# Performance work log

Hardware: AMD Instinct MI355X
Metric: run time of the kernel (lower is better)

Reference implementation:

```python
import jax, jax.numpy as jnp
import numpy as np

D = 256      # input_size == output_size
H = 8        # head_count
DH = D // H  # dim per head


def setup_inputs() -> dict:
    key = jax.random.key(0)
    ks = jax.random.split(key, 11)
    s = 1.0 / np.sqrt(D)
    inp = {
        "x": jax.random.normal(ks[0], (4, 2048, D), dtype=jnp.float32),
        "Wq": jax.random.normal(ks[1], (D, D), dtype=jnp.float32) * s,
        "bq": jnp.zeros((D,), jnp.float32),
        "Wk": jax.random.normal(ks[2], (D, D), dtype=jnp.float32) * s,
        "bk": jnp.zeros((D,), jnp.float32),
        "Wv": jax.random.normal(ks[3], (D, D), dtype=jnp.float32) * s,
        "bv": jnp.zeros((D,), jnp.float32),
        "Wo": jax.random.normal(ks[4], (D, D), dtype=jnp.float32) * s,
        "bo": jnp.zeros((D,), jnp.float32),
        "Wc": jax.random.normal(ks[5], (D, D), dtype=jnp.float32) * s,
        "bc": jnp.zeros((D,), jnp.float32),
    }
    return inp


def _split_heads(t):
    b, n, _ = t.shape
    return t.reshape(b, n, H, DH).transpose(0, 2, 1, 3)  # b h n dh


def reference(x, Wq, bq, Wk, bk, Wv, bv, Wo, bo, Wc, bc):
    # Multi-head self-attention over all nodes (complete graph)
    q = _split_heads(x @ Wq + bq)
    k = _split_heads(x @ Wk + bk)
    v = _split_heads(x @ Wv + bv)
    scale = 1.0 / jnp.sqrt(jnp.asarray(DH, x.dtype))
    scores = jnp.einsum("bhqd,bhkd->bhqk", q * scale, k)
    attn = jax.nn.softmax(scores, axis=-1)  # attn dropout = identity (eval)
    ctx = jnp.einsum("bhqk,bhkd->bhqd", attn, v)
    b, _, n, _ = ctx.shape
    ctx = ctx.transpose(0, 2, 1, 3).reshape(b, n, D)
    ctx = ctx @ Wo + bo  # MHA output projection
    # linear_context + dropout (identity in eval) + residual
    out = x + (ctx @ Wc + bc)
    return out
```

## Files before the change

### kernel.cpp

```cpp
#include <hip/hip_runtime.h>

#define DMODEL 256
#define HEADS 8
#define DHEAD 32
#define NSEQ 2048
#define BATCH 4
#define MTOT (BATCH*NSEQ)

typedef __bf16 bf16x8 __attribute__((ext_vector_type(8)));
typedef float f32x4 __attribute__((ext_vector_type(4)));

#define CS 0.25507282111989365f

__device__ __forceinline__ unsigned short f2bf(float f) {
    union { float f; unsigned int u; } v; v.f = f;
    unsigned int u = v.u;
    unsigned int r = u + 0x7FFFu + ((u >> 16) & 1u);
    return (unsigned short)(r >> 16);
}

__device__ __forceinline__ unsigned pkbf(float a, float b) {
    union { __bf16 h[2]; unsigned u; } t;
    t.h[0] = (__bf16)a; t.h[1] = (__bf16)b;
    return t.u;
}

__device__ __forceinline__ f32x4 mfma16(bf16x8 a, bf16x8 b, f32x4 c) {
    return __builtin_amdgcn_mfma_f32_16x16x32_bf16(a, b, c, 0, 0, 0);
}

#define GLD16(g, l) __builtin_amdgcn_global_load_lds( \
    (const __attribute__((address_space(1))) unsigned int*)(g), \
    (__attribute__((address_space(3))) unsigned int*)(l), 16, 0, 0)

__global__ __launch_bounds__(256) void prep_kernel(
    const float* __restrict__ x,
    const float* __restrict__ Wq, const float* __restrict__ Wk,
    const float* __restrict__ Wv, const float* __restrict__ Wo,
    const float* __restrict__ Wc,
    const float* __restrict__ bq, const float* __restrict__ bk,
    const float* __restrict__ bv, const float* __restrict__ bo,
    const float* __restrict__ bc,
    unsigned short* __restrict__ xbf,
    unsigned short* __restrict__ Wt,
    float* __restrict__ bcat,
    unsigned short* __restrict__ Woct,
    float* __restrict__ bocf)
{
    const int tid = threadIdx.x;
    if (blockIdx.x < 257) {
        int k = blockIdx.x;
        int n = tid;
        const float* arow = (k < 256) ? (Wo + k * 256) : bo;
        float a0 = 0.f, a1 = 0.f, a2 = 0.f, a3 = 0.f;
#pragma unroll 4
        for (int j = 0; j < 256; j += 4) {
            a0 = fmaf(arow[j],     Wc[j * 256 + n],       a0);
            a1 = fmaf(arow[j + 1], Wc[(j + 1) * 256 + n], a1);
            a2 = fmaf(arow[j + 2], Wc[(j + 2) * 256 + n], a2);
            a3 = fmaf(arow[j + 3], Wc[(j + 3) * 256 + n], a3);
        }
        float acc = (a0 + a1) + (a2 + a3);
        if (k < 256) Woct[n * 256 + k] = f2bf(acc);
        else         bocf[n] = acc + bc[n];
        return;
    }
    if (blockIdx.x < 2305) {
        int idx = (blockIdx.x - 257) * 256 + tid;
        float4 v = reinterpret_cast<const float4*>(x)[idx];
        ushort4 o;
        o.x = f2bf(v.x); o.y = f2bf(v.y); o.z = f2bf(v.z); o.w = f2bf(v.w);
        reinterpret_cast<ushort4*>(xbf)[idx] = o;
        return;
    }
    if (blockIdx.x < 2385) {
        __shared__ unsigned short Lt[64 * 72];
        const int bb = blockIdx.x - 2305;
        const int wid = tid >> 6, lane = tid & 63;
        const int n0 = (bb >> 2) * 64, k0 = (bb & 3) * 64;
        const float* Wsrc; int col0;
        if (n0 < 256)       { Wsrc = Wq; col0 = n0; }
        else if (n0 < 512)  { Wsrc = Wk; col0 = n0 - 256; }
        else if (n0 < 768)  { Wsrc = Wv; col0 = n0 - 512; }
        else if (n0 < 1024) { Wsrc = Wo; col0 = n0 - 768; }
        else                { Wsrc = Wc; col0 = n0 - 1024; }
#pragma unroll
        for (int r = 0; r < 16; ++r) {
            int k = k0 + wid * 16 + r;
            Lt[lane * 72 + wid * 16 + r] = f2bf(Wsrc[k * 256 + col0 + lane]);
        }
        __syncthreads();
#pragma unroll
        for (int c = tid; c < 512; c += 256) {
            int row = c >> 3, seg = c & 7;
            *reinterpret_cast<bf16x8*>(Wt + (n0 + row) * 256 + k0 + seg * 8) =
                *reinterpret_cast<const bf16x8*>(Lt + row * 72 + seg * 8);
        }
        return;
    }
    int t = (blockIdx.x - 2385) * 256 + tid;
    if (t < 1280) {
        float v;
        if (t < 256)       v = bq[t];
        else if (t < 512)  v = bk[t - 256];
        else if (t < 768)  v = bv[t - 512];
        else if (t < 1024) v = bo[t - 768];
        else               v = bc[t - 1024];
        bcat[t] = v;
    }
}

__global__ __launch_bounds__(256) void gemm_qkv(
    const unsigned short* __restrict__ A,
    const unsigned short* __restrict__ Wt,
    const float* __restrict__ bias,
    unsigned short* __restrict__ outQ,
    unsigned short* __restrict__ outK,
    unsigned short* __restrict__ outVt)
{
    __shared__ __align__(16) unsigned short Bl[64 * 256];
    const int tid = threadIdx.x;
    const int wid = tid >> 6;
    const int lane = tid & 63;
    const int lo = lane & 15, hi = lane >> 4;
    const int m0 = blockIdx.x * 128 + wid * 32;
    const int n0 = blockIdx.y * 64;

#pragma unroll
    for (int j = 0; j < 8; ++j) {
        int chunkbase = (j * 4 + wid) * 64;
        int chunk = chunkbase + lane;
        int row = chunk >> 5, Jp = chunk & 31;
        int J = (Jp & 24) | ((Jp ^ row) & 7);
        GLD16(Wt + (n0 + row) * 256 + J * 8, Bl + chunkbase * 8);
    }
    asm volatile("s_waitcnt vmcnt(0)" ::: "memory");
    __syncthreads();

    const unsigned short* arow0 = A + (m0 + lo) * 256 + hi * 8;
    f32x4 acc[2][4] = {};
#pragma unroll
    for (int s = 0; s < 8; ++s) {
        bf16x8 a0 = *reinterpret_cast<const bf16x8*>(arow0 + s * 32);
        bf16x8 a1 = *reinterpret_cast<const bf16x8*>(arow0 + 16 * 256 + s * 32);
        int Jp = ((s >> 1) << 3) | ((((s & 1) << 2) + hi) ^ (lo & 7));
#pragma unroll
        for (int n = 0; n < 4; ++n) {
            bf16x8 b = *reinterpret_cast<const bf16x8*>(
                Bl + (n * 16 + lo) * 256 + Jp * 8);
            acc[0][n] = mfma16(a0, b, acc[0][n]);
            acc[1][n] = mfma16(a1, b, acc[1][n]);
        }
    }

    const int type = blockIdx.y >> 2;
    const int m0b = blockIdx.x * 128;
    unsigned short* Lb = Bl;
    __syncthreads();
    if (type < 2) {
#pragma unroll
        for (int mf = 0; mf < 2; ++mf)
#pragma unroll
        for (int n = 0; n < 4; ++n) {
            float bs = bias[n0 + n * 16 + lo];
#pragma unroll
            for (int i = 0; i < 4; ++i) {
                float val = acc[mf][n][i] + bs;
                if (type == 0) val *= CS;
                Lb[(wid * 32 + mf * 16 + hi * 4 + i) * 72 + n * 16 + lo] = f2bf(val);
            }
        }
    } else {
#pragma unroll
        for (int mf = 0; mf < 2; ++mf)
#pragma unroll
        for (int n = 0; n < 4; ++n) {
            float bs = bias[n0 + n * 16 + lo];
            uint2 pk;
            pk.x = pkbf(acc[mf][n][0] + bs, acc[mf][n][1] + bs);
            pk.y = pkbf(acc[mf][n][2] + bs, acc[mf][n][3] + bs);
            *reinterpret_cast<uint2*>(
                Lb + (n * 16 + lo) * 136 + wid * 32 + mf * 16 + hi * 4) = pk;
        }
    }
    __syncthreads();
    if (type < 2) {
        unsigned short* outP = (type == 0) ? outQ : outK;
#pragma unroll
        for (int r = 0; r < 4; ++r) {
            int cid = r * 256 + tid;
            int m_l = cid >> 3, seg = cid & 7;
            bf16x8 chunk = *reinterpret_cast<const bf16x8*>(Lb + m_l * 72 + seg * 8);
            int m = m0b + m_l, gc = n0 + seg * 8;
            int b = m >> 11, nn = m & 2047, hh = (gc >> 5) & 7, dh = gc & 31;
            *reinterpret_cast<bf16x8*>(
                outP + (((b * 8) + hh) * 2048 + nn) * 32 + dh) = chunk;
        }
    } else {
#pragma unroll
        for (int r = 0; r < 4; ++r) {
            int cid = r * 256 + tid;
            int gcl = cid >> 4, seg = cid & 15;
            const unsigned short* src = Lb + gcl * 136 + seg * 8;
            uint2 lo4 = *reinterpret_cast<const uint2*>(src);
            uint2 hi4 = *reinterpret_cast<const uint2*>(src + 4);
            int gc = n0 + gcl, m = m0b + seg * 8;
            int b = m >> 11, nn = m & 2047, hh = (gc >> 5) & 7, dh = gc & 31;
            int pos0 = (nn & ~63) | (nn & 32) | ((nn & 8) << 1) | ((nn & 16) >> 2);
            unsigned short* dst = outVt + (((b * 8) + hh) * 32 + dh) * 2048;
            *reinterpret_cast<uint2*>(dst + pos0)     = lo4;
            *reinterpret_cast<uint2*>(dst + pos0 + 8) = hi4;
        }
    }
}

__global__ __launch_bounds__(256, 4) void attn_kernel(
    const unsigned short* __restrict__ Q,
    const unsigned short* __restrict__ K,
    const unsigned short* __restrict__ Vt,
    unsigned short* __restrict__ ctx)
{
    __shared__ __align__(16) char smem[32768];

    const int tid = threadIdx.x;
    const int wid = tid >> 6;
    const int lane = tid & 63;
    const int lo = lane & 15, hi = lane >> 4;

    const int bid = blockIdx.x;
    const int bh = ((bid >> 7) << 3) | (bid & 7);
    const int qt = (bid >> 3) & 15;
    const int q0 = qt * 128 + wid * 32;

    const unsigned short* Qb = Q + bh * (NSEQ * 32);
    const unsigned short* Kb = K + bh * (NSEQ * 32);
    const unsigned short* Vb = Vt + bh * (32 * NSEQ);

    bf16x8 qfA = *reinterpret_cast<const bf16x8*>(Qb + (q0 + lo) * 32 + hi * 8);
    bf16x8 qfB = *reinterpret_cast<const bf16x8*>(Qb + (q0 + 16 + lo) * 32 + hi * 8);

    const int lt = tid;
    const unsigned short* ksrc0 = Kb + (2 * (lt >> 3) + ((lt >> 2) & 1)) * 32
                                     + ((lt & 3) ^ ((lt >> 3) & 3)) * 8;
    const unsigned short* ksrc1 = ksrc0 + 64 * 32;
    const unsigned short* vsrc0 = Vb + (lt >> 3) * NSEQ
                                     + ((lt & 7) ^ ((lt >> 3) & 7)) * 8;
    const unsigned short* vsrc1 = vsrc0 + 64;
    char* kdst = smem + lt * 16;
    char* vdst = smem + 16384 + lt * 16;

    f32x4 o0A = {}, o1A = {}, odA = {};
    f32x4 o0B = {}, o1B = {}, odB = {};
    const f32x4 z = {};
    const int prs = lo & 7;
    const int kxor = (hi ^ ((lo >> 1) & 3)) * 8;

    union { unsigned u[4]; bf16x8 v; } ones;
    ones.u[0] = 0x3F803F80u; ones.u[1] = 0x3F803F80u;
    ones.u[2] = 0x3F803F80u; ones.u[3] = 0x3F803F80u;

#define STAGE_T(tt, buf) do { \
    GLD16(ksrc0 + (tt) * 4096, kdst + (buf) * 8192); \
    GLD16(ksrc1 + (tt) * 4096, kdst + (buf) * 8192 + 4096); \
    GLD16(vsrc0 + (tt) * 128,  vdst + (buf) * 8192); \
    GLD16(vsrc1 + (tt) * 128,  vdst + (buf) * 8192 + 4096); \
} while (0)

#define PVKK(S0, S1, T0, T1, A0, A1) do { \
    union { unsigned u[4]; bf16x8 v; } pbA; \
    pbA.u[0] = pkbf(__builtin_amdgcn_exp2f(S0[0]), __builtin_amdgcn_exp2f(S0[1])); \
    pbA.u[1] = pkbf(__builtin_amdgcn_exp2f(S0[2]), __builtin_amdgcn_exp2f(S0[3])); \
    pbA.u[2] = pkbf(__builtin_amdgcn_exp2f(S1[0]), __builtin_amdgcn_exp2f(S1[1])); \
    pbA.u[3] = pkbf(__builtin_amdgcn_exp2f(S1[2]), __builtin_amdgcn_exp2f(S1[3])); \
    union { unsigned u[4]; bf16x8 v; } pbB; \
    pbB.u[0] = pkbf(__builtin_amdgcn_exp2f(T0[0]), __builtin_amdgcn_exp2f(T0[1])); \
    pbB.u[1] = pkbf(__builtin_amdgcn_exp2f(T0[2]), __builtin_amdgcn_exp2f(T0[3])); \
    pbB.u[2] = pkbf(__builtin_amdgcn_exp2f(T1[0]), __builtin_amdgcn_exp2f(T1[1])); \
    pbB.u[3] = pkbf(__builtin_amdgcn_exp2f(T1[2]), __builtin_amdgcn_exp2f(T1[3])); \
    o0A = mfma16(A0, pbA.v, o0A); \
    o1A = mfma16(A1, pbA.v, o1A); \
    odA = mfma16(ones.v, pbA.v, odA); \
    o0B = mfma16(A0, pbB.v, o0B); \
    o1B = mfma16(A1, pbB.v, o1B); \
    odB = mfma16(ones.v, pbB.v, odB); \
} while (0)

    STAGE_T(0, 0);
    asm volatile("s_waitcnt vmcnt(0)" ::: "memory");
    __builtin_amdgcn_s_barrier();
    __builtin_amdgcn_sched_barrier(0);

    int cur = 0;
    for (int t = 0; t < 16; ++t) {
        if (t < 15) STAGE_T(t + 1, cur ^ 1);
        const unsigned short* Kc = (const unsigned short*)(smem + cur * 8192);
        const unsigned short* Vc = (const unsigned short*)(smem + 16384 + cur * 8192);

        __builtin_amdgcn_s_setprio(1);
#pragma unroll
        for (int h2 = 0; h2 < 2; ++h2) {
            const unsigned short* Kh = Kc + h2 * 2048;
            const unsigned short* Vh = Vc + h2 * 2048;
            f32x4 sA[4], sB[4];
#pragma unroll
            for (int c = 0; c < 4; ++c) {
                bf16x8 kf = *reinterpret_cast<const bf16x8*>(
                    Kh + (c * 16 + lo) * 32 + kxor);
                sA[c] = mfma16(kf, qfA, z);
                sB[c] = mfma16(kf, qfB, z);
            }
#pragma unroll
            for (int kk = 0; kk < 2; ++kk) {
                int sw = ((4 * kk + hi) ^ prs) * 8;
                bf16x8 a0 = *reinterpret_cast<const bf16x8*>(Vh + lo * 64 + sw);
                bf16x8 a1 = *reinterpret_cast<const bf16x8*>(Vh + (16 + lo) * 64 + sw);
                PVKK(sA[2 * kk], sA[2 * kk + 1], sB[2 * kk], sB[2 * kk + 1], a0, a1);
            }
        }
        __builtin_amdgcn_s_setprio(0);

        if (t < 15) {
            asm volatile("s_waitcnt vmcnt(0)" ::: "memory");
            __builtin_amdgcn_s_barrier();
            __builtin_amdgcn_sched_barrier(0);
            cur ^= 1;
        }
    }

    float invA = 1.0f / odA[0];
    float invB = 1.0f / odB[0];
    const int b = bh >> 3, h = bh & 7;
    unsigned short* dstA = ctx + (size_t)((b * 2048 + q0 + lo)) * 256 + h * 32;
    unsigned short* dstB = dstA + 16 * 256;
    ushort4 w0, w1;
    w0.x = f2bf(o0A[0] * invA); w0.y = f2bf(o0A[1] * invA);
    w0.z = f2bf(o0A[2] * invA); w0.w = f2bf(o0A[3] * invA);
    w1.x = f2bf(o1A[0] * invA); w1.y = f2bf(o1A[1] * invA);
    w1.z = f2bf(o1A[2] * invA); w1.w = f2bf(o1A[3] * invA);
    *reinterpret_cast<ushort4*>(dstA + hi * 4)      = w0;
    *reinterpret_cast<ushort4*>(dstA + 16 + hi * 4) = w1;
    w0.x = f2bf(o0B[0] * invB); w0.y = f2bf(o0B[1] * invB);
    w0.z = f2bf(o0B[2] * invB); w0.w = f2bf(o0B[3] * invB);
    w1.x = f2bf(o1B[0] * invB); w1.y = f2bf(o1B[1] * invB);
    w1.z = f2bf(o1B[2] * invB); w1.w = f2bf(o1B[3] * invB);
    *reinterpret_cast<ushort4*>(dstB + hi * 4)      = w0;
    *reinterpret_cast<ushort4*>(dstB + 16 + hi * 4) = w1;
#undef STAGE_T
#undef PVKK
}

__global__ __launch_bounds__(256) void gemm_ctx(
    const unsigned short* __restrict__ A,
    const unsigned short* __restrict__ Wt,
    const float* __restrict__ boc,
    const float* __restrict__ xres,
    float* __restrict__ outF)
{
    __shared__ __align__(16) unsigned short Bl[64 * 256];
    const int tid = threadIdx.x;
    const int wid = tid >> 6;
    const int lane = tid & 63;
    const int lo = lane & 15, hi = lane >> 4;
    const int m0 = blockIdx.x * 128 + wid * 32;
    const int n0 = blockIdx.y * 64;

#pragma unroll
    for (int j = 0; j < 8; ++j) {
        int chunkbase = (j * 4 + wid) * 64;
        int chunk = chunkbase + lane;
        int row = chunk >> 5, Jp = chunk & 31;
        int J = (Jp & 24) | ((Jp ^ row) & 7);
        GLD16(Wt + (n0 + row) * 256 + J * 8, Bl + chunkbase * 8);
    }
    asm volatile("s_waitcnt vmcnt(0)" ::: "memory");
    __syncthreads();

    const unsigned short* arow0 = A + (m0 + lo) * 256 + hi * 8;
    f32x4 acc[2][4] = {};
#pragma unroll
    for (int s = 0; s < 8; ++s) {
        bf16x8 a0 = *reinterpret_cast<const bf16x8*>(arow0 + s * 32);
        bf16x8 a1 = *reinterpret_cast<const bf16x8*>(arow0 + 16 * 256 + s * 32);
        int Jp = ((s >> 1) << 3) | ((((s & 1) << 2) + hi) ^ (lo & 7));
#pragma unroll
        for (int n = 0; n < 4; ++n) {
            bf16x8 b = *reinterpret_cast<const bf16x8*>(
                Bl + (n * 16 + lo) * 256 + Jp * 8);
            acc[0][n] = mfma16(a0, b, acc[0][n]);
            acc[1][n] = mfma16(a1, b, acc[1][n]);
        }
    }
#pragma unroll
    for (int mf = 0; mf < 2; ++mf) {
        const int row_base = m0 + mf * 16 + hi * 4;
#pragma unroll
        for (int n = 0; n < 4; ++n) {
            int gc = n0 + n * 16 + lo;
            float bs = boc[gc];
#pragma unroll
            for (int i = 0; i < 4; ++i)
                outF[(row_base + i) * 256 + gc] =
                    xres[(row_base + i) * 256 + gc] + acc[mf][n][i] + bs;
        }
    }
}

extern "C" void kernel_launch(void* const* d_in, const int* in_sizes, int n_in,
                              void* d_out, int out_size, void* d_ws, size_t ws_size,
                              hipStream_t stream) {
    const float* x  = (const float*)d_in[0];
    const float* Wq = (const float*)d_in[1];
    const float* bq = (const float*)d_in[2];
    const float* Wk = (const float*)d_in[3];
    const float* bk = (const float*)d_in[4];
    const float* Wv = (const float*)d_in[5];
    const float* bv = (const float*)d_in[6];
    const float* Wo = (const float*)d_in[7];
    const float* bo = (const float*)d_in[8];
    const float* Wc = (const float*)d_in[9];
    const float* bc = (const float*)d_in[10];
    float* out = (float*)d_out;

    char* p = (char*)d_ws;
    unsigned short* xbf  = (unsigned short*)p;  p += (size_t)MTOT * DMODEL * 2;
    unsigned short* Wt   = (unsigned short*)p;  p += (size_t)1280 * 256 * 2;
    float* bcat          = (float*)p;           p += (size_t)1280 * 4;
    unsigned short* Qw   = (unsigned short*)p;  p += (size_t)32 * 2048 * 32 * 2;
    unsigned short* Kw   = (unsigned short*)p;  p += (size_t)32 * 2048 * 32 * 2;
    unsigned short* Vtw  = (unsigned short*)p;  p += (size_t)32 * 32 * 2048 * 2;
    unsigned short* ctx  = (unsigned short*)p;  p += (size_t)MTOT * DMODEL * 2;
    unsigned short* Woct = (unsigned short*)p;  p += (size_t)256 * 256 * 2;
    float* bocf          = (float*)p;           p += (size_t)256 * 4;

    prep_kernel<<<2390, 256, 0, stream>>>(x, Wq, Wk, Wv, Wo, Wc,
                                          bq, bk, bv, bo, bc,
                                          xbf, Wt, bcat, Woct, bocf);
    gemm_qkv<<<dim3(64, 12), 256, 0, stream>>>(xbf, Wt, bcat, Qw, Kw, Vtw);
    attn_kernel<<<512, 256, 0, stream>>>(Qw, Kw, Vtw, ctx);
    gemm_ctx<<<dim3(64, 4), 256, 0, stream>>>(ctx, Woct, bocf, x, out);
}
```

Baseline: 59.49 us.

## Split attention KV range across wave pairs and widen per-wave query tiles

Each wave now handles 64 queries (four 16-row groups) instead of 32, so every K/V fragment read from LDS feeds twice as many MFMAs. The two wave pairs in a block each cover half of the key sequence, staged into separate LDS regions, and their partial outputs and denominators are merged through LDS at the end. This cuts LDS read traffic per FLOP and halves the loop trip count. In exchange it doubles LDS use to 64KB, lowers the occupancy bound from 4 to 2 blocks, raises register pressure, and adds a cross-wave combine step.

```diff
diff --git a/kernel.cpp b/kernel.cpp
--- a/kernel.cpp
+++ b/kernel.cpp
@@ -214,43 +214,52 @@
     }
 }
 
-__global__ __launch_bounds__(256, 4) void attn_kernel(
+__global__ __launch_bounds__(256, 2) void attn_kernel(
     const unsigned short* __restrict__ Q,
     const unsigned short* __restrict__ K,
     const unsigned short* __restrict__ Vt,
     unsigned short* __restrict__ ctx)
 {
-    __shared__ __align__(16) char smem[32768];
+    __shared__ __align__(16) char smem[65536];
 
     const int tid = threadIdx.x;
     const int wid = tid >> 6;
     const int lane = tid & 63;
     const int lo = lane & 15, hi = lane >> 4;
+    const int qsub = wid & 1;
+    const int half = wid >> 1;
 
     const int bid = blockIdx.x;
     const int bh = ((bid >> 7) << 3) | (bid & 7);
     const int qt = (bid >> 3) & 15;
-    const int q0 = qt * 128 + wid * 32;
+    const int q0 = qt * 128 + qsub * 64;
 
     const unsigned short* Qb = Q + bh * (NSEQ * 32);
-    const unsigned short* Kb = K + bh * (NSEQ * 32);
-    const unsigned short* Vb = Vt + bh * (32 * NSEQ);
-
-    bf16x8 qfA = *reinterpret_cast<const bf16x8*>(Qb + (q0 + lo) * 32 + hi * 8);
-    bf16x8 qfB = *reinterpret_cast<const bf16x8*>(Qb + (q0 + 16 + lo) * 32 + hi * 8);
-
-    const int lt = tid;
-    const unsigned short* ksrc0 = Kb + (2 * (lt >> 3) + ((lt >> 2) & 1)) * 32
-                                     + ((lt & 3) ^ ((lt >> 3) & 3)) * 8;
-    const unsigned short* ksrc1 = ksrc0 + 64 * 32;
-    const unsigned short* vsrc0 = Vb + (lt >> 3) * NSEQ
-                                     + ((lt & 7) ^ ((lt >> 3) & 7)) * 8;
-    const unsigned short* vsrc1 = vsrc0 + 64;
-    char* kdst = smem + lt * 16;
-    char* vdst = smem + 16384 + lt * 16;
-
-    f32x4 o0A = {}, o1A = {}, odA = {};
-    f32x4 o0B = {}, o1B = {}, odB = {};
+    const unsigned short* Kh0 = K + bh * (NSEQ * 32) + (half * 1024) * 32;
+    const unsigned short* Vh0 = Vt + bh * (32 * NSEQ) + half * 1024;
+
+    bf16x8 qf[4];
+#pragma unroll
+    for (int g = 0; g < 4; ++g)
+        qf[g] = *reinterpret_cast<const bf16x8*>(
+            Qb + (q0 + g * 16 + lo) * 32 + hi * 8);
+
+    const int lt2 = tid & 127;
+    const int cA = lt2, cB = lt2 + 128;
+    const unsigned short* kA0 = Kh0 + (2 * (cA >> 3) + ((cA >> 2) & 1)) * 32
+                                    + ((cA & 3) ^ ((cA >> 3) & 3)) * 8;
+    const unsigned short* kA1 = Kh0 + (2 * (cB >> 3) + ((cB >> 2) & 1)) * 32
+                                    + ((cB & 3) ^ ((cB >> 3) & 3)) * 8;
+    const unsigned short* vA0 = Vh0 + (cA >> 3) * NSEQ
+                                    + ((cA & 7) ^ ((cA >> 3) & 7)) * 8;
+    const unsigned short* vA1 = Vh0 + (cB >> 3) * NSEQ
+                                    + ((cB & 7) ^ ((cB >> 3) & 7)) * 8;
+    char* kd0 = smem + half * 16384 + lt2 * 16;
+    char* kd1 = kd0 + 2048;
+    char* vd0 = smem + 32768 + half * 16384 + lt2 * 16;
+    char* vd1 = vd0 + 2048;
+
+    f32x4 o0[4] = {}, o1[4] = {}, od[4] = {};
     const f32x4 z = {};
     const int prs = lo & 7;
     const int kxor = (hi ^ ((lo >> 1) & 3)) * 8;
@@ -260,29 +269,14 @@
     ones.u[2] = 0x3F803F80u; ones.u[3] = 0x3F803F80u;
 
 #define STAGE_T(tt, buf) do { \
-    GLD16(ksrc0 + (tt) * 4096, kdst + (buf) * 8192); \
-    GLD16(ksrc1 + (tt) * 4096, kdst + (buf) * 8192 + 4096); \
-    GLD16(vsrc0 + (tt) * 128,  vdst + (buf) * 8192); \
-    GLD16(vsrc1 + (tt) * 128,  vdst + (buf) * 8192 + 4096); \
-} while (0)
-
-#define PVKK(S0, S1, T0, T1, A0, A1) do { \
-    union { unsigned u[4]; bf16x8 v; } pbA; \
-    pbA.u[0] = pkbf(__builtin_amdgcn_exp2f(S0[0]), __builtin_amdgcn_exp2f(S0[1])); \
-    pbA.u[1] = pkbf(__builtin_amdgcn_exp2f(S0[2]), __builtin_amdgcn_exp2f(S0[3])); \
-    pbA.u[2] = pkbf(__builtin_amdgcn_exp2f(S1[0]), __builtin_amdgcn_exp2f(S1[1])); \
-    pbA.u[3] = pkbf(__builtin_amdgcn_exp2f(S1[2]), __builtin_amdgcn_exp2f(S1[3])); \
-    union { unsigned u[4]; bf16x8 v; } pbB; \
-    pbB.u[0] = pkbf(__builtin_amdgcn_exp2f(T0[0]), __builtin_amdgcn_exp2f(T0[1])); \
-    pbB.u[1] = pkbf(__builtin_amdgcn_exp2f(T0[2]), __builtin_amdgcn_exp2f(T0[3])); \
-    pbB.u[2] = pkbf(__builtin_amdgcn_exp2f(T1[0]), __builtin_amdgcn_exp2f(T1[1])); \
-    pbB.u[3] = pkbf(__builtin_amdgcn_exp2f(T1[2]), __builtin_amdgcn_exp2f(T1[3])); \
-    o0A = mfma16(A0, pbA.v, o0A); \
-    o1A = mfma16(A1, pbA.v, o1A); \
-    odA = mfma16(ones.v, pbA.v, odA); \
-    o0B = mfma16(A0, pbB.v, o0B); \
-    o1B = mfma16(A1, pbB.v, o1B); \
-    odB = mfma16(ones.v, pbB.v, odB); \
+    GLD16(kA0 + (tt) * 4096,        kd0 + (buf) * 8192); \
+    GLD16(kA0 + (tt) * 4096 + 2048, kd0 + (buf) * 8192 + 4096); \
+    GLD16(kA1 + (tt) * 4096,        kd1 + (buf) * 8192); \
+    GLD16(kA1 + (tt) * 4096 + 2048, kd1 + (buf) * 8192 + 4096); \
+    GLD16(vA0 + (tt) * 128,         vd0 + (buf) * 8192); \
+    GLD16(vA0 + (tt) * 128 + 64,    vd0 + (buf) * 8192 + 4096); \
+    GLD16(vA1 + (tt) * 128,         vd1 + (buf) * 8192); \
+    GLD16(vA1 + (tt) * 128 + 64,    vd1 + (buf) * 8192 + 4096); \
 } while (0)
 
     STAGE_T(0, 0);
@@ -291,35 +285,53 @@
     __builtin_amdgcn_sched_barrier(0);
 
     int cur = 0;
-    for (int t = 0; t < 16; ++t) {
-        if (t < 15) STAGE_T(t + 1, cur ^ 1);
-        const unsigned short* Kc = (const unsigned short*)(smem + cur * 8192);
-        const unsigned short* Vc = (const unsigned short*)(smem + 16384 + cur * 8192);
+    for (int t = 0; t < 8; ++t) {
+        if (t < 7) STAGE_T(t + 1, cur ^ 1);
+        const unsigned short* Kc =
+            (const unsigned short*)(smem + half * 16384 + cur * 8192);
+        const unsigned short* Vc =
+            (const unsigned short*)(smem + 32768 + half * 16384 + cur * 8192);
 
         __builtin_amdgcn_s_setprio(1);
 #pragma unroll
         for (int h2 = 0; h2 < 2; ++h2) {
             const unsigned short* Kh = Kc + h2 * 2048;
             const unsigned short* Vh = Vc + h2 * 2048;
-            f32x4 sA[4], sB[4];
+            f32x4 s[4][4];
 #pragma unroll
             for (int c = 0; c < 4; ++c) {
                 bf16x8 kf = *reinterpret_cast<const bf16x8*>(
                     Kh + (c * 16 + lo) * 32 + kxor);
-                sA[c] = mfma16(kf, qfA, z);
-                sB[c] = mfma16(kf, qfB, z);
+#pragma unroll
+                for (int g = 0; g < 4; ++g)
+                    s[g][c] = mfma16(kf, qf[g], z);
             }
 #pragma unroll
             for (int kk = 0; kk < 2; ++kk) {
                 int sw = ((4 * kk + hi) ^ prs) * 8;
                 bf16x8 a0 = *reinterpret_cast<const bf16x8*>(Vh + lo * 64 + sw);
                 bf16x8 a1 = *reinterpret_cast<const bf16x8*>(Vh + (16 + lo) * 64 + sw);
-                PVKK(sA[2 * kk], sA[2 * kk + 1], sB[2 * kk], sB[2 * kk + 1], a0, a1);
+#pragma unroll
+                for (int g = 0; g < 4; ++g) {
+                    const f32x4 s0 = s[g][2 * kk], s1 = s[g][2 * kk + 1];
+                    union { unsigned u[4]; bf16x8 v; } pb;
+                    pb.u[0] = pkbf(__builtin_amdgcn_exp2f(s0[0]),
+                                   __builtin_amdgcn_exp2f(s0[1]));
+                    pb.u[1] = pkbf(__builtin_amdgcn_exp2f(s0[2]),
+                                   __builtin_amdgcn_exp2f(s0[3]));
+                    pb.u[2] = pkbf(__builtin_amdgcn_exp2f(s1[0]),
+                                   __builtin_amdgcn_exp2f(s1[1]));
+                    pb.u[3] = pkbf(__builtin_amdgcn_exp2f(s1[2]),
+                                   __builtin_amdgcn_exp2f(s1[3]));
+                    o0[g] = mfma16(a0, pb.v, o0[g]);
+                    o1[g] = mfma16(a1, pb.v, o1[g]);
+                    od[g] = mfma16(ones.v, pb.v, od[g]);
+                }
             }
         }
         __builtin_amdgcn_s_setprio(0);
 
-        if (t < 15) {
+        if (t < 7) {
             asm volatile("s_waitcnt vmcnt(0)" ::: "memory");
             __builtin_amdgcn_s_barrier();
             __builtin_amdgcn_sched_barrier(0);
@@ -327,26 +339,38 @@
         }
     }
 
-    float invA = 1.0f / odA[0];
-    float invB = 1.0f / odB[0];
-    const int b = bh >> 3, h = bh & 7;
-    unsigned short* dstA = ctx + (size_t)((b * 2048 + q0 + lo)) * 256 + h * 32;
-    unsigned short* dstB = dstA + 16 * 256;
-    ushort4 w0, w1;
-    w0.x = f2bf(o0A[0] * invA); w0.y = f2bf(o0A[1] * invA);
-    w0.z = f2bf(o0A[2] * invA); w0.w = f2bf(o0A[3] * invA);
-    w1.x = f2bf(o1A[0] * invA); w1.y = f2bf(o1A[1] * invA);
-    w1.z = f2bf(o1A[2] * invA); w1.w = f2bf(o1A[3] * invA);
-    *reinterpret_cast<ushort4*>(dstA + hi * 4)      = w0;
-    *reinterpret_cast<ushort4*>(dstA + 16 + hi * 4) = w1;
-    w0.x = f2bf(o0B[0] * invB); w0.y = f2bf(o0B[1] * invB);
-    w0.z = f2bf(o0B[2] * invB); w0.w = f2bf(o0B[3] * invB);
-    w1.x = f2bf(o1B[0] * invB); w1.y = f2bf(o1B[1] * invB);
-    w1.z = f2bf(o1B[2] * invB); w1.w = f2bf(o1B[3] * invB);
-    *reinterpret_cast<ushort4*>(dstB + hi * 4)      = w0;
-    *reinterpret_cast<ushort4*>(dstB + 16 + hi * 4) = w1;
+    float* comb = (float*)smem;
+    const int cidx = (qsub * 64 + lane) * 48;
+    __syncthreads();
+    if (half) {
+#pragma unroll
+        for (int g = 0; g < 4; ++g) {
+            *reinterpret_cast<f32x4*>(comb + cidx + g * 12)     = o0[g];
+            *reinterpret_cast<f32x4*>(comb + cidx + g * 12 + 4) = o1[g];
+            comb[cidx + g * 12 + 8] = od[g][0];
+        }
+    }
+    __syncthreads();
+    if (!half) {
+        const int b = bh >> 3, h = bh & 7;
+#pragma unroll
+        for (int g = 0; g < 4; ++g) {
+            f32x4 p0 = *reinterpret_cast<const f32x4*>(comb + cidx + g * 12);
+            f32x4 p1 = *reinterpret_cast<const f32x4*>(comb + cidx + g * 12 + 4);
+            float inv = 1.0f / (od[g][0] + comb[cidx + g * 12 + 8]);
+            f32x4 r0 = o0[g] + p0, r1 = o1[g] + p1;
+            unsigned short* dst = ctx
+                + (size_t)((b * 2048 + q0 + g * 16 + lo)) * 256 + h * 32;
+            ushort4 w0, w1;
+            w0.x = f2bf(r0[0] * inv); w0.y = f2bf(r0[1] * inv);
+            w0.z = f2bf(r0[2] * inv); w0.w = f2bf(r0[3] * inv);
+            w1.x = f2bf(r1[0] * inv); w1.y = f2bf(r1[1] * inv);
+            w1.z = f2bf(r1[2] * inv); w1.w = f2bf(r1[3] * inv);
+            *reinterpret_cast<ushort4*>(dst + hi * 4)      = w0;
+            *reinterpret_cast<ushort4*>(dst + 16 + hi * 4) = w1;
+        }
+    }
 #undef STAGE_T
-#undef PVKK
 }
 
 __global__ __launch_bounds__(256) void gemm_ctx(
```

Result: no change. 58.88 us (-1.0%).
